# Kernel tuning notes

Hardware: AMD Instinct MI355X
Metric: run time of the kernel (lower is better)

## Reference

```python
import jax, jax.numpy as jnp
import numpy as np
from jax import lax

DIM = 2048
K = 3


def rms_norm(x):
    eps = jnp.asarray(jnp.finfo(x.dtype).eps, x.dtype)
    var = jnp.mean(jnp.square(x), axis=-1, keepdims=True)
    return x * lax.rsqrt(var + eps)


def causal_dwconv1d(y, w, b, dilation):
    # y: [B, S, D]; w: [D, 1, K]; depthwise causal conv along S
    yc = jnp.transpose(y, (0, 2, 1))  # [B, D, S]
    pad = (K - 1) * dilation
    out = lax.conv_general_dilated(
        yc, w.astype(yc.dtype),
        window_strides=(1,),
        padding=[(pad, 0)],
        rhs_dilation=(dilation,),
        dimension_numbers=('NCH', 'OIH', 'NCH'),
        feature_group_count=DIM,
    )
    out = out + b.astype(yc.dtype)[None, :, None]
    return jnp.transpose(out, (0, 2, 1))  # [B, S, D]


def setup_inputs() -> dict:
    key = jax.random.key(0)
    ks = jax.random.split(key, 4)
    B, S, D = 4, 4096, DIM
    x = jax.random.normal(ks[0], (B, S, D), dtype=jnp.float32)
    W_expand = jax.random.normal(ks[1], (3 * D, D), dtype=jnp.float32) * (1.0 / np.sqrt(D))
    conv_w = jax.random.normal(ks[2], (D, 1, K), dtype=jnp.float32) * (1.0 / K)
    conv_b = jnp.zeros((D,), dtype=jnp.float32)
    W_proj = jax.random.normal(ks[3], (D, D), dtype=jnp.float32) * (1.0 / np.sqrt(D))
    conv_scale = jnp.ones((D,), dtype=jnp.float32)
    return {"x": x, "W_expand": W_expand, "conv_w": conv_w, "conv_b": conv_b,
            "W_proj": W_proj, "conv_scale": conv_scale, "dilation": 1}


def reference(x, W_expand, conv_w, conv_b, W_proj, conv_scale, dilation):
    h = jnp.einsum('bsd,ed->bse', rms_norm(x), W_expand.astype(x.dtype))
    B_gate, C_gate, z = jnp.split(h, 3, axis=-1)
    y = B_gate * z  # squared_gate=False
    y = causal_dwconv1d(y, conv_w, conv_b, dilation)
    o = C_gate * y
    o = jnp.einsum('bsd,ed->bse', o, W_proj.astype(x.dtype))
    return x + conv_scale.astype(x.dtype)[None, None, :] * o
```

## Files before the change

### kernel.cpp

```cpp
#include <hip/hip_runtime.h>
#include <hip/hip_bf16.h>
#include <stdint.h>

typedef __bf16 bf16;
typedef __bf16 bf16x8 __attribute__((ext_vector_type(8)));
typedef __bf16 bf16x4 __attribute__((ext_vector_type(4)));
typedef float  floatx4 __attribute__((ext_vector_type(4)));

#define DIMD 2048
#define BATB 4
#define SEQS 4096
#define MTOT (BATB*SEQS)

__device__ __forceinline__ void gload_lds16(const bf16* g, bf16* l) {
    __builtin_amdgcn_global_load_lds(
        (const __attribute__((address_space(1))) void*)g,
        (__attribute__((address_space(3))) void*)l,
        16, 0, 0);
}

__global__ __launch_bounds__(256) void f2bf_k(const float* __restrict__ src,
                                              bf16* __restrict__ dst, int n) {
    int i = (blockIdx.x * 256 + threadIdx.x) * 4;
    if (i >= n) return;
    float4 v = *(const float4*)&src[i];
    bf16x4 o;
    o[0] = (bf16)v.x; o[1] = (bf16)v.y; o[2] = (bf16)v.z; o[3] = (bf16)v.w;
    *(bf16x4*)&dst[i] = o;
}

__global__ __launch_bounds__(256) void rmsnorm_k(const float* __restrict__ x,
                                                 bf16* __restrict__ xn) {
    const int row = blockIdx.x;
    const int tid = threadIdx.x;
    const float* xr = x + (size_t)row * DIMD;
    float4 a = *(const float4*)&xr[tid * 8];
    float4 b = *(const float4*)&xr[tid * 8 + 4];
    float s = a.x*a.x + a.y*a.y + a.z*a.z + a.w*a.w
            + b.x*b.x + b.y*b.y + b.z*b.z + b.w*b.w;
    #pragma unroll
    for (int off = 32; off > 0; off >>= 1) s += __shfl_down(s, off);
    __shared__ float red[4];
    if ((tid & 63) == 0) red[tid >> 6] = s;
    __syncthreads();
    float tot = red[0] + red[1] + red[2] + red[3];
    float sc = rsqrtf(tot * (1.0f / DIMD) + 1.1920929e-07f);
    bf16x8 o;
    o[0] = (bf16)(a.x * sc); o[1] = (bf16)(a.y * sc);
    o[2] = (bf16)(a.z * sc); o[3] = (bf16)(a.w * sc);
    o[4] = (bf16)(b.x * sc); o[5] = (bf16)(b.y * sc);
    o[6] = (bf16)(b.z * sc); o[7] = (bf16)(b.w * sc);
    *(bf16x8*)&xn[(size_t)row * DIMD + tid * 8] = o;
}

__global__ __launch_bounds__(256) void gateconv_k(const bf16* __restrict__ h,
                                                  const float* __restrict__ cw,
                                                  const float* __restrict__ cb,
                                                  bf16* __restrict__ o,
                                                  const int* __restrict__ dil_p) {
    int gid = blockIdx.x * 256 + threadIdx.x;
    int m = gid >> 9;
    int d = (gid & 511) << 2;
    int s = m & (SEQS - 1);
    int dil = dil_p[0];
    const bf16* hr = h + (size_t)m * (3 * DIMD);

    bf16x4 Cv = *(const bf16x4*)&hr[DIMD + d];
    bf16x4 B0 = *(const bf16x4*)&hr[d];
    bf16x4 Z0 = *(const bf16x4*)&hr[2 * DIMD + d];
    float y0[4], y1[4], y2[4];
    #pragma unroll
    for (int j = 0; j < 4; ++j) y0[j] = (float)B0[j] * (float)Z0[j];
    if (s >= dil) {
        const bf16* h1 = hr - (size_t)dil * 3 * DIMD;
        bf16x4 B1 = *(const bf16x4*)&h1[d];
        bf16x4 Z1 = *(const bf16x4*)&h1[2 * DIMD + d];
        #pragma unroll
        for (int j = 0; j < 4; ++j) y1[j] = (float)B1[j] * (float)Z1[j];
    } else {
        #pragma unroll
        for (int j = 0; j < 4; ++j) y1[j] = 0.0f;
    }
    if (s >= 2 * dil) {
        const bf16* h2 = hr - (size_t)(2 * dil) * 3 * DIMD;
        bf16x4 B2 = *(const bf16x4*)&h2[d];
        bf16x4 Z2 = *(const bf16x4*)&h2[2 * DIMD + d];
        #pragma unroll
        for (int j = 0; j < 4; ++j) y2[j] = (float)B2[j] * (float)Z2[j];
    } else {
        #pragma unroll
        for (int j = 0; j < 4; ++j) y2[j] = 0.0f;
    }
    bf16x4 ov;
    #pragma unroll
    for (int j = 0; j < 4; ++j) {
        float w0 = cw[(d + j) * 3 + 0];
        float w1 = cw[(d + j) * 3 + 1];
        float w2 = cw[(d + j) * 3 + 2];
        float conv = w0 * y2[j] + w1 * y1[j] + w2 * y0[j] + cb[d + j];
        ov[j] = (bf16)((float)Cv[j] * conv);
    }
    *(bf16x4*)&o[(size_t)m * DIMD + d] = ov;
}

template<int RESID>
__global__ __launch_bounds__(256) void gemm_bt(const bf16* __restrict__ A,
                                               const bf16* __restrict__ B,
                                               bf16* __restrict__ Hout,
                                               float* __restrict__ Fout,
                                               const float* __restrict__ resid,
                                               const float* __restrict__ scale,
                                               int M, int N, int K) {
    constexpr int BM = 128, BN = 128, BK = 64;
    __shared__ __align__(16) bf16 As[BM * BK];
    __shared__ __align__(16) bf16 Bs[BN * BK];
    const int tid = threadIdx.x;
    const int wave = tid >> 6;
    const int lane = tid & 63;
    const int quad = lane >> 4;
    const int col16 = lane & 15;
    const int m0 = blockIdx.y * BM;
    const int n0 = blockIdx.x * BN;
    const int wm = (wave >> 1) * 64;
    const int wn = (wave & 1) * 64;

    const bf16* aptr[4];
    const bf16* bptr[4];
    bf16* alds[4];
    bf16* blds[4];
    #pragma unroll
    for (int j = 0; j < 4; ++j) {
        int idx = j * 256 + wave * 64 + lane;
        int row = idx >> 3;
        int ck = ((idx ^ row) & 7) * 8;
        aptr[j] = A + (size_t)(m0 + row) * K + ck;
        bptr[j] = B + (size_t)(n0 + row) * K + ck;
        int ubase = (j * 256 + wave * 64) * 8;
        alds[j] = As + ubase;
        blds[j] = Bs + ubase;
    }

    floatx4 acc[4][4];
    #pragma unroll
    for (int i = 0; i < 4; ++i)
        #pragma unroll
        for (int j = 0; j < 4; ++j) acc[i][j] = (floatx4)0.0f;

    const int rswiz = col16 & 7;

    for (int k0 = 0; k0 < K; k0 += BK) {
        #pragma unroll
        for (int j = 0; j < 4; ++j) gload_lds16(aptr[j] + k0, alds[j]);
        #pragma unroll
        for (int j = 0; j < 4; ++j) gload_lds16(bptr[j] + k0, blds[j]);
        __syncthreads();
        #pragma unroll
        for (int kk = 0; kk < BK; kk += 32) {
            const int slot = ((quad + (kk >> 5) * 4) ^ rswiz) * 8;
            bf16x8 af[4], bfr[4];
            #pragma unroll
            for (int mi = 0; mi < 4; ++mi)
                af[mi] = *(const bf16x8*)&As[(wm + mi * 16 + col16) * BK + slot];
            #pragma unroll
            for (int ni = 0; ni < 4; ++ni)
                bfr[ni] = *(const bf16x8*)&Bs[(wn + ni * 16 + col16) * BK + slot];
            #pragma unroll
            for (int mi = 0; mi < 4; ++mi)
                #pragma unroll
                for (int ni = 0; ni < 4; ++ni)
                    acc[mi][ni] = __builtin_amdgcn_mfma_f32_16x16x32_bf16(
                        af[mi], bfr[ni], acc[mi][ni], 0, 0, 0);
        }
        __syncthreads();
    }

    #pragma unroll
    for (int mi = 0; mi < 4; ++mi) {
        #pragma unroll
        for (int ni = 0; ni < 4; ++ni) {
            int c = n0 + wn + ni * 16 + col16;
            int rbase = m0 + wm + mi * 16 + quad * 4;
            #pragma unroll
            for (int r = 0; r < 4; ++r) {
                size_t off = (size_t)(rbase + r) * N + c;
                float v = acc[mi][ni][r];
                if (RESID) {
                    Fout[off] = resid[off] + scale[c] * v;
                } else {
                    Hout[off] = (bf16)v;
                }
            }
        }
    }
}

extern "C" void kernel_launch(void* const* d_in, const int* in_sizes, int n_in,
                              void* d_out, int out_size, void* d_ws, size_t ws_size,
                              hipStream_t stream) {
    const float* x  = (const float*)d_in[0];
    const float* We = (const float*)d_in[1];
    const float* cw = (const float*)d_in[2];
    const float* cb = (const float*)d_in[3];
    const float* Wp = (const float*)d_in[4];
    const float* cs = (const float*)d_in[5];
    const int*   dil = (const int*)d_in[6];

    char* ws = (char*)d_ws;
    bf16* xn  = (bf16*)ws;
    bf16* Web = (bf16*)(ws + 67108864);
    bf16* Wpb = (bf16*)(ws + 67108864 + 25165824);
    bf16* h   = (bf16*)(ws + 100663296);

    f2bf_k<<<(3 * DIMD * DIMD / 4 + 255) / 256, 256, 0, stream>>>(We, Web, 3 * DIMD * DIMD);
    f2bf_k<<<(DIMD * DIMD / 4 + 255) / 256, 256, 0, stream>>>(Wp, Wpb, DIMD * DIMD);
    rmsnorm_k<<<MTOT, 256, 0, stream>>>(x, xn);
    gemm_bt<0><<<dim3(3 * DIMD / 128, MTOT / 128), 256, 0, stream>>>(
        xn, Web, h, nullptr, nullptr, nullptr, MTOT, 3 * DIMD, DIMD);
    gateconv_k<<<(MTOT * (DIMD / 4)) / 256, 256, 0, stream>>>(h, cw, cb, xn , dil);
    gemm_bt<1><<<dim3(DIMD / 128, MTOT / 128), 256, 0, stream>>>(
        xn , Wpb, nullptr, (float*)d_out, x, cs, MTOT, DIMD, DIMD);
}
```

Measured before the change: 991.6 us.

## Rewrite GEMM as 256x256 double-buffered 8-wave pipelined kernel with block remap

Replaces the 128x128 single-buffered GEMM with a 256x256 tile computed by 512 threads (8 waves). It double-buffers LDS and interleaves global-to-LDS staging of the next K tiles with MFMA work, using explicit waitcnt, barriers and setprio. It also remaps block IDs in an XCD-aware way for cache locality. The goal is to hide memory latency and raise reuse per tile, at the cost of 128KB of LDS per block, higher register pressure and fragile hand-tuned synchronization.

After: 829.9 us. -16.3%, faster.

```diff
diff --git a/kernel.cpp b/kernel.cpp
--- a/kernel.cpp
+++ b/kernel.cpp
@@ -11,6 +11,13 @@
 #define BATB 4
 #define SEQS 4096
 #define MTOT (BATB*SEQS)
+
+#define BAR()   __builtin_amdgcn_s_barrier()
+#define LGKM0() asm volatile("s_waitcnt lgkmcnt(0)" ::: "memory")
+#define LGKM8() asm volatile("s_waitcnt lgkmcnt(8)" ::: "memory")
+#define VMC6()  asm volatile("s_waitcnt vmcnt(6)" ::: "memory")
+#define VMC0()  asm volatile("s_waitcnt vmcnt(0)" ::: "memory")
+#define SCHED0() __builtin_amdgcn_sched_barrier(0)
 
 __device__ __forceinline__ void gload_lds16(const bf16* g, bf16* l) {
     __builtin_amdgcn_global_load_lds(
@@ -104,94 +111,198 @@
 }
 
 template<int RESID>
-__global__ __launch_bounds__(256) void gemm_bt(const bf16* __restrict__ A,
-                                               const bf16* __restrict__ B,
-                                               bf16* __restrict__ Hout,
-                                               float* __restrict__ Fout,
-                                               const float* __restrict__ resid,
-                                               const float* __restrict__ scale,
-                                               int M, int N, int K) {
-    constexpr int BM = 128, BN = 128, BK = 64;
-    __shared__ __align__(16) bf16 As[BM * BK];
-    __shared__ __align__(16) bf16 Bs[BN * BK];
+__global__ __launch_bounds__(512, 2) void gemm_bt(const bf16* __restrict__ A,
+                                                  const bf16* __restrict__ B,
+                                                  bf16* __restrict__ Hout,
+                                                  float* __restrict__ Fout,
+                                                  const float* __restrict__ resid,
+                                                  const float* __restrict__ scale,
+                                                  int M, int N, int K) {
+    __shared__ __align__(16) bf16 smem[2][32768];
     const int tid = threadIdx.x;
     const int wave = tid >> 6;
     const int lane = tid & 63;
     const int quad = lane >> 4;
     const int col16 = lane & 15;
-    const int m0 = blockIdx.y * BM;
-    const int n0 = blockIdx.x * BN;
-    const int wm = (wave >> 1) * 64;
-    const int wn = (wave & 1) * 64;
-
-    const bf16* aptr[4];
-    const bf16* bptr[4];
-    bf16* alds[4];
-    bf16* blds[4];
-    #pragma unroll
-    for (int j = 0; j < 4; ++j) {
-        int idx = j * 256 + wave * 64 + lane;
-        int row = idx >> 3;
-        int ck = ((idx ^ row) & 7) * 8;
-        aptr[j] = A + (size_t)(m0 + row) * K + ck;
-        bptr[j] = B + (size_t)(n0 + row) * K + ck;
-        int ubase = (j * 256 + wave * 64) * 8;
-        alds[j] = As + ubase;
-        blds[j] = Bs + ubase;
-    }
-
-    floatx4 acc[4][4];
-    #pragma unroll
-    for (int i = 0; i < 4; ++i)
-        #pragma unroll
-        for (int j = 0; j < 4; ++j) acc[i][j] = (floatx4)0.0f;
-
-    const int rswiz = col16 & 7;
-
-    for (int k0 = 0; k0 < K; k0 += BK) {
-        #pragma unroll
-        for (int j = 0; j < 4; ++j) gload_lds16(aptr[j] + k0, alds[j]);
-        #pragma unroll
-        for (int j = 0; j < 4; ++j) gload_lds16(bptr[j] + k0, blds[j]);
-        __syncthreads();
-        #pragma unroll
-        for (int kk = 0; kk < BK; kk += 32) {
-            const int slot = ((quad + (kk >> 5) * 4) ^ rswiz) * 8;
-            bf16x8 af[4], bfr[4];
+
+    const int nx   = (int)gridDim.x;
+    const int nwg  = nx * (int)gridDim.y;
+    const int orig = (int)blockIdx.y * nx + (int)blockIdx.x;
+    const int lin  = (orig & 7) * (nwg >> 3) + (orig >> 3);
+    const int n0 = (lin % nx) * 256;
+    const int m0 = (lin / nx) * 256;
+
+    const int wm = (wave >> 2) * 128;
+    const int wn = (wave & 3) * 64;
+
+    const int srow = tid >> 3;
+    const int cs   = (tid & 7) ^ (srow & 7);
+    const bf16* aSrc = A + (size_t)(m0 + srow) * K + cs * 8;
+    const bf16* bSrc = B + (size_t)(n0 + srow) * K + cs * 8;
+    const int stbase = wave * 512;
+    const size_t K64  = (size_t)K * 64;
+    const size_t K128 = (size_t)K * 128;
+
+    const int rsw = col16 & 7;
+    const int ard = (wm + col16) * 64;
+    const int brd = (wn + col16) * 64;
+    const int sl0 = ((0 + quad) ^ rsw) * 8;
+    const int sl1 = ((4 + quad) ^ rsw) * 8;
+
+    floatx4 acc[4][2][4];
+    #pragma unroll
+    for (int q = 0; q < 4; ++q)
+        #pragma unroll
+        for (int f = 0; f < 2; ++f)
             #pragma unroll
-            for (int mi = 0; mi < 4; ++mi)
-                af[mi] = *(const bf16x8*)&As[(wm + mi * 16 + col16) * BK + slot];
+            for (int n = 0; n < 4; ++n) acc[q][f][n] = (floatx4)0.0f;
+
+    auto stage = [&](const bf16* src, bf16* dstBase, int t, int h) {
+        const bf16* s = src + (size_t)h * K128 + (size_t)t * 64;
+        bf16* d = dstBase + h * 8192 + stbase;
+        gload_lds16(s, d);
+        gload_lds16(s + K64, d + 4096);
+    };
+    auto lda2 = [&](bf16x8 (&q)[2][2], const bf16* Asb, int f0) {
+        #pragma unroll
+        for (int f = 0; f < 2; ++f) {
+            const bf16* p = Asb + ard + (f0 + f) * (16 * 64);
+            q[f][0] = *(const bf16x8*)(p + sl0);
+            q[f][1] = *(const bf16x8*)(p + sl1);
+        }
+    };
+    auto ldb4 = [&](bf16x8 (&q)[4][2], const bf16* Bsb) {
+        #pragma unroll
+        for (int n = 0; n < 4; ++n) {
+            const bf16* p = Bsb + brd + n * (16 * 64);
+            q[n][0] = *(const bf16x8*)(p + sl0);
+            q[n][1] = *(const bf16x8*)(p + sl1);
+        }
+    };
+    auto mm = [&](floatx4 (&ac)[2][4], bf16x8 (&a)[2][2], bf16x8 (&b)[4][2]) {
+        __builtin_amdgcn_s_setprio(1);
+        #pragma unroll
+        for (int f = 0; f < 2; ++f)
             #pragma unroll
-            for (int ni = 0; ni < 4; ++ni)
-                bfr[ni] = *(const bf16x8*)&Bs[(wn + ni * 16 + col16) * BK + slot];
+            for (int n = 0; n < 4; ++n) {
+                ac[f][n] = __builtin_amdgcn_mfma_f32_16x16x32_bf16(a[f][0], b[n][0], ac[f][n], 0, 0, 0);
+                ac[f][n] = __builtin_amdgcn_mfma_f32_16x16x32_bf16(a[f][1], b[n][1], ac[f][n], 0, 0, 0);
+            }
+        __builtin_amdgcn_s_setprio(0);
+    };
+
+    const int NT = K >> 6;
+
+    stage(aSrc, smem[0],         0, 0);
+    stage(aSrc, smem[0],         0, 1);
+    stage(bSrc, smem[0] + 16384, 0, 0);
+    stage(bSrc, smem[0] + 16384, 0, 1);
+    stage(bSrc, smem[1] + 16384, 1, 0);
+    stage(bSrc, smem[1] + 16384, 1, 1);
+    stage(aSrc, smem[1],         1, 0);
+    VMC6();
+    BAR();
+
+    for (int t = 0; t < NT - 2; ++t) {
+        const int b = t & 1;
+        const bf16* Asb = smem[b];
+        const bf16* Bsb = smem[b] + 16384;
+        bf16* Asw = smem[b];
+        bf16* Bsw = smem[b] + 16384;
+        bf16* Aso = smem[b ^ 1];
+        bf16x8 bfr[4][2], A0[2][2], A1[2][2], A2[2][2], A3[2][2];
+        ldb4(bfr, Bsb);
+        lda2(A0, Asb, 0);
+        stage(aSrc, Aso, t + 1, 1);
+        LGKM8();
+        BAR(); LGKM0(); SCHED0();
+        mm(acc[0], A0, bfr);
+        BAR();
+        lda2(A1, Asb, 2);
+        lda2(A2, Asb, 4);
+        stage(bSrc, Bsw, t + 2, 0);
+        BAR(); LGKM0(); SCHED0();
+        mm(acc[1], A1, bfr);
+        BAR();
+        lda2(A3, Asb, 6);
+        stage(bSrc, Bsw, t + 2, 1);
+        BAR(); LGKM0(); SCHED0();
+        mm(acc[2], A2, bfr);
+        BAR();
+        stage(aSrc, Asw, t + 2, 0);
+        VMC6();
+        BAR();
+        mm(acc[3], A3, bfr);
+        BAR();
+    }
+    {
+        const int t = NT - 2;
+        const int b = t & 1;
+        const bf16* Asb = smem[b];
+        const bf16* Bsb = smem[b] + 16384;
+        bf16* Aso = smem[b ^ 1];
+        bf16x8 bfr[4][2], A0[2][2], A1[2][2], A2[2][2], A3[2][2];
+        ldb4(bfr, Bsb);
+        lda2(A0, Asb, 0);
+        stage(aSrc, Aso, t + 1, 1);
+        LGKM8();
+        BAR(); LGKM0(); SCHED0();
+        mm(acc[0], A0, bfr);
+        BAR();
+        lda2(A1, Asb, 2);
+        lda2(A2, Asb, 4);
+        BAR(); LGKM0(); SCHED0();
+        mm(acc[1], A1, bfr);
+        BAR();
+        lda2(A3, Asb, 6);
+        BAR(); LGKM0(); SCHED0();
+        mm(acc[2], A2, bfr);
+        BAR();
+        VMC0();
+        BAR();
+        mm(acc[3], A3, bfr);
+        BAR();
+    }
+    {
+        const int b = (NT - 1) & 1;
+        const bf16* Asb = smem[b];
+        const bf16* Bsb = smem[b] + 16384;
+        bf16x8 bfr[4][2], A0[2][2], A1[2][2], A2[2][2], A3[2][2];
+        ldb4(bfr, Bsb);
+        lda2(A0, Asb, 0);
+        BAR(); LGKM0(); SCHED0();
+        mm(acc[0], A0, bfr);
+        BAR();
+        lda2(A1, Asb, 2);
+        lda2(A2, Asb, 4);
+        BAR(); LGKM0(); SCHED0();
+        mm(acc[1], A1, bfr);
+        BAR();
+        lda2(A3, Asb, 6);
+        BAR(); LGKM0(); SCHED0();
+        mm(acc[2], A2, bfr);
+        mm(acc[3], A3, bfr);
+    }
+
+    #pragma unroll
+    for (int q2 = 0; q2 < 4; ++q2)
+        #pragma unroll
+        for (int f = 0; f < 2; ++f)
             #pragma unroll
-            for (int mi = 0; mi < 4; ++mi)
+            for (int n = 0; n < 4; ++n) {
+                const int c  = n0 + wn + n * 16 + col16;
+                const int rb = m0 + wm + (q2 * 2 + f) * 16 + quad * 4;
                 #pragma unroll
-                for (int ni = 0; ni < 4; ++ni)
-                    acc[mi][ni] = __builtin_amdgcn_mfma_f32_16x16x32_bf16(
-                        af[mi], bfr[ni], acc[mi][ni], 0, 0, 0);
-        }
-        __syncthreads();
-    }
-
-    #pragma unroll
-    for (int mi = 0; mi < 4; ++mi) {
-        #pragma unroll
-        for (int ni = 0; ni < 4; ++ni) {
-            int c = n0 + wn + ni * 16 + col16;
-            int rbase = m0 + wm + mi * 16 + quad * 4;
-            #pragma unroll
-            for (int r = 0; r < 4; ++r) {
-                size_t off = (size_t)(rbase + r) * N + c;
-                float v = acc[mi][ni][r];
-                if (RESID) {
-                    Fout[off] = resid[off] + scale[c] * v;
-                } else {
-                    Hout[off] = (bf16)v;
+                for (int r = 0; r < 4; ++r) {
+                    size_t off = (size_t)(rb + r) * N + c;
+                    float v = acc[q2][f][n][r];
+                    if (RESID) {
+                        Fout[off] = resid[off] + scale[c] * v;
+                    } else {
+                        Hout[off] = (bf16)v;
+                    }
                 }
             }
-        }
-    }
 }
 
 extern "C" void kernel_launch(void* const* d_in, const int* in_sizes, int n_in,
@@ -214,9 +325,9 @@
     f2bf_k<<<(3 * DIMD * DIMD / 4 + 255) / 256, 256, 0, stream>>>(We, Web, 3 * DIMD * DIMD);
     f2bf_k<<<(DIMD * DIMD / 4 + 255) / 256, 256, 0, stream>>>(Wp, Wpb, DIMD * DIMD);
     rmsnorm_k<<<MTOT, 256, 0, stream>>>(x, xn);
-    gemm_bt<0><<<dim3(3 * DIMD / 128, MTOT / 128), 256, 0, stream>>>(
+    gemm_bt<0><<<dim3(3 * DIMD / 256, MTOT / 256), 512, 0, stream>>>(
         xn, Web, h, nullptr, nullptr, nullptr, MTOT, 3 * DIMD, DIMD);
     gateconv_k<<<(MTOT * (DIMD / 4)) / 256, 256, 0, stream>>>(h, cw, cb, xn , dil);
-    gemm_bt<1><<<dim3(DIMD / 128, MTOT / 128), 256, 0, stream>>>(
+    gemm_bt<1><<<dim3(DIMD / 256, MTOT / 256), 512, 0, stream>>>(
         xn , Wpb, nullptr, (float*)d_out, x, cs, MTOT, DIMD, DIMD);
 }
```
